# Optimization experiments

Measured on AMD Instinct MI355X. Metric: run time of the kernel, lower is better.

## Reference

```python
import jax, jax.numpy as jnp
import numpy as np

LN_EPS = 1e-5


def conv2d(x, w, b, stride, pad):
    # x: NCHW, w: OIHW
    y = jax.lax.conv_general_dilated(
        x, w, (stride, stride), [(pad, pad), (pad, pad)],
        dimension_numbers=("NCHW", "OIHW", "NCHW"))
    return y + b[None, :, None, None]


def gdn(x, gamma, beta):
    # y_c = x_c / sqrt(beta_c + sum_j gamma_cj * x_j^2)  (1x1 conv on x^2)
    norm = jnp.einsum("bchw,dc->bdhw", x * x, gamma) + beta[None, :, None, None]
    return x / jnp.sqrt(norm)


def layernorm(x, w, b):
    mu = jnp.mean(x, axis=-1, keepdims=True)
    var = jnp.var(x, axis=-1, keepdims=True)
    return (x - mu) / jnp.sqrt(var + LN_EPS) * w + b


def setup_inputs() -> dict:
    key = jax.random.key(0)
    ks = jax.random.split(key, 16)
    r = lambda i, shape: (jax.random.normal(ks[i], shape) * 0.02).astype(jnp.float32)
    N, M, K, D = 128, 192, 192, 128
    return {
        "x_p": jax.random.normal(ks[0], (4, 16, 3, 64, 64), jnp.float32),
        "y_g": jax.random.normal(ks[1], (64, K, 32), jnp.float32),
        "conv1_w": r(2, (N, 3, 5, 5)), "conv1_b": jnp.zeros((N,), jnp.float32),
        "gamma1": (0.1 * jnp.eye(N) + 1e-3).astype(jnp.float32), "beta1": jnp.ones((N,), jnp.float32),
        "conv2_w": r(3, (N, N, 5, 5)), "conv2_b": jnp.zeros((N,), jnp.float32),
        "gamma2": (0.1 * jnp.eye(N) + 1e-3).astype(jnp.float32), "beta2": jnp.ones((N,), jnp.float32),
        "conv3_w": r(4, (M, N, 3, 3)), "conv3_b": jnp.zeros((M,), jnp.float32),
        "ln_q_w": jnp.ones((M,), jnp.float32), "ln_q_b": jnp.zeros((M,), jnp.float32),
        "ln_kv_w": jnp.ones((K,), jnp.float32), "ln_kv_b": jnp.zeros((K,), jnp.float32),
        "ln_out_w": jnp.ones((M,), jnp.float32), "ln_out_b": jnp.zeros((M,), jnp.float32),
        "Wq": r(5, (D, M)), "Wk": r(6, (D, K)), "v_w": r(7, (1, D)),
        "Wv": r(8, (M, K)), "out_w": r(9, (M, M)), "out_b": jnp.zeros((M,), jnp.float32),
    }


def reference(x_p, y_g, conv1_w, conv1_b, gamma1, beta1, conv2_w, conv2_b,
              gamma2, beta2, conv3_w, conv3_b, ln_q_w, ln_q_b, ln_kv_w, ln_kv_b,
              ln_out_w, ln_out_b, Wq, Wk, v_w, Wv, out_w, out_b):
    B, P, C, Hp, Wp = x_p.shape
    x = x_p.reshape(B * P, C, Hp, Wp)
    # local encoder: conv s2 -> GDN -> conv s2 -> GDN -> conv s1 k3
    x = gdn(conv2d(x, conv1_w, conv1_b, 2, 2), gamma1, beta1)
    x = gdn(conv2d(x, conv2_w, conv2_b, 2, 2), gamma2, beta2)
    y_local = conv2d(x, conv3_w, conv3_b, 1, 1)          # (BP, M, h, w)
    BP, M, h, w = y_local.shape
    q = y_local.reshape(BP, M, h * w).transpose(0, 2, 1)  # (BP, Tq, M)
    kv = y_g.reshape(BP, y_g.shape[1], -1).transpose(0, 2, 1)  # (BP, Tk, K)
    q = layernorm(q, ln_q_w, ln_q_b)
    kv = layernorm(kv, ln_kv_w, ln_kv_b)
    # Bahdanau additive attention
    q_proj = jnp.einsum("bqm,dm->bqd", q, Wq)            # (BP, Tq, D)
    k_proj = jnp.einsum("bkc,dc->bkd", kv, Wk)           # (BP, Tk, D)
    energy = jnp.einsum("bqkd,d->bqk",
                        jnp.tanh(q_proj[:, :, None, :] + k_proj[:, None, :, :]),
                        v_w[0])                           # (BP, Tq, Tk)
    alpha = jax.nn.softmax(energy, axis=-1)
    v_proj = jnp.einsum("bkc,mc->bkm", kv, Wv)           # (BP, Tk, M)
    context = jnp.einsum("bqk,bkm->bqm", alpha, v_proj)
    context = jnp.einsum("bqm,nm->bqn", context, out_w) + out_b
    fused = layernorm(q + context, ln_out_w, ln_out_b)
    return fused.transpose(0, 2, 1).reshape(BP, M, h, w)
```

## Files before the change

### kernel.cpp

```cpp
#include <hip/hip_runtime.h>
#include <cstddef>
#include <cstdint>


typedef __bf16 bf16x8 __attribute__((ext_vector_type(8)));
typedef float floatx4 __attribute__((ext_vector_type(4)));
typedef unsigned short ushortT;
typedef unsigned short ushort8v __attribute__((ext_vector_type(8)));

#if __has_builtin(__builtin_amdgcn_exp2f)
#define EXP2F(x) __builtin_amdgcn_exp2f(x)
#else
#define EXP2F(x) exp2f(x)
#endif
#if __has_builtin(__builtin_amdgcn_rcpf)
#define RCPF(x) __builtin_amdgcn_rcpf(x)
#else
#define RCPF(x) (1.f / (x))
#endif

__device__ __forceinline__ ushortT f2bf(float f) {
  unsigned u = __builtin_bit_cast(unsigned, f);
  unsigned r = (u + 0x7FFFu + ((u >> 16) & 1u)) >> 16;
  return (ushortT)r;
}
__device__ __forceinline__ float bf2f(ushortT u) {
  return __builtin_bit_cast(float, ((unsigned)u) << 16);
}

static constexpr size_t OFF_T1BF = 0;
static constexpr size_t OFF_X2BF = 4194304;
static constexpr size_t OFF_T2BF = 8388608;
static constexpr size_t OFF_X3BF = 9437184;
static constexpr size_t OFF_QRAW = 10485760;
static constexpr size_t OFF_WBQ  = 21299200;
static constexpr size_t OFF_WBK  = 21311488;
static constexpr size_t OFF_WBV  = 21323776;
static constexpr size_t OFF_WBO  = 21342208;
static constexpr size_t OFF_WT2  = 26079232;
static constexpr size_t OFF_WT3  = 26284032;
static constexpr size_t OFF_WC1  = 26394624;
static constexpr size_t OFF_GB1  = 26406912;
static constexpr size_t OFF_GB2  = 26415104;

__device__ __constant__ int d_TWI2[4][9] = {{ 0, 2, 4,10,12,14,20,22,24},
                                            { 1, 3,11,13,21,23, 0, 0, 0},
                                            { 5, 7, 9,15,17,19, 0, 0, 0},
                                            { 6, 8,16,18, 0, 0, 0, 0, 0}};
__device__ __constant__ int d_NT2[4] = {9, 6, 6, 4};

__device__ void dev_convw3(const float* w, ushortT* wt, int mode, int total,
                           int idx) {
  if (idx >= total) return;
  int j    = idx & 7;
  int om   = (idx >> 3) & 63;
  int kg   = (idx >> 9) & 3;
  int slab = idx >> 11;
  int mt, s, tap, T;
  if (mode == 0) {
    int ph;
    if (slab < 72) ph = 0; else if (slab < 120) ph = 1;
    else if (slab < 168) ph = 2; else ph = 3;
    const int st[4] = {0, 72, 120, 168};
    const int ns[4] = {36, 24, 24, 16};
    int rel = slab - st[ph];
    mt = rel / ns[ph]; s = rel % ns[ph];
    tap = d_TWI2[ph][s >> 2]; T = 25;
  } else {
    mt = slab / 36; s = slab % 36; tap = s >> 2; T = 9;
  }
  int cc = s & 3;
  int c  = cc * 32 + kg * 8 + j;
  int oc = mt * 64 + om;
  wt[idx] = f2bf(w[(size_t)(oc * 128 + c) * T + tap]);
}

__device__ void dev_convw1(const float* w, ushortT* wt, int idx) {
  if (idx >= 20480) return;
  int k    = idx & 31;
  int oc   = (idx >> 5) & 127;
  int slab = idx >> 12;
  int ph, i;
  if (slab < 2) { ph = 0; i = slab; } else { ph = slab - 1; i = 0; }
  int kg = k >> 3, jj = k & 7;
  int tidx = i * 8 + jj;
  float val = 0.f;
  if (kg < 3 && tidx < d_NT2[ph]) {
    int tap = d_TWI2[ph][tidx];
    val = w[(size_t)(oc * 3 + kg) * 25 + tap];
  }
  wt[idx] = f2bf(val);
}

__device__ void dev_wcast(const float* w, ushortT* wb, int total, float scale,
                          int idx) {
  if (idx < total) wb[idx] = f2bf(w[idx] * scale);
}

__global__ __launch_bounds__(256) void prep_kernel(
    const float* __restrict__ conv2_w, ushortT* __restrict__ wt2,
    const float* __restrict__ conv3_w, ushortT* __restrict__ wt3,
    const float* __restrict__ conv1_w, ushortT* __restrict__ wc1,
    const float* __restrict__ Wq, ushortT* __restrict__ wbq,
    const float* __restrict__ Wk, ushortT* __restrict__ wbk,
    const float* __restrict__ Wv, ushortT* __restrict__ wbv,
    const float* __restrict__ out_w, ushortT* __restrict__ wbo,
    const float* __restrict__ gamma1, ushortT* __restrict__ gb1,
    const float* __restrict__ gamma2, ushortT* __restrict__ gb2) {
  constexpr float C2LE = 2.88539008177792681f;
  int blk = blockIdx.x, tid = threadIdx.x;
  if (blk < 1600)      dev_convw3(conv2_w, wt2, 0, 409600, blk * 256 + tid);
  else if (blk < 2464) dev_convw3(conv3_w, wt3, 1, 221184, (blk - 1600) * 256 + tid);
  else if (blk < 2544) dev_convw1(conv1_w, wc1, (blk - 2464) * 256 + tid);
  else if (blk < 2640) dev_wcast(Wq, wbq, 24576, C2LE, (blk - 2544) * 256 + tid);
  else if (blk < 2736) dev_wcast(Wk, wbk, 24576, C2LE, (blk - 2640) * 256 + tid);
  else if (blk < 2880) dev_wcast(Wv, wbv, 36864, 1.f, (blk - 2736) * 256 + tid);
  else if (blk < 3024) dev_wcast(out_w, wbo, 36864, 1.f, (blk - 2880) * 256 + tid);
  else if (blk < 3088) dev_wcast(gamma1, gb1, 16384, 1.f, (blk - 3024) * 256 + tid);
  else                 dev_wcast(gamma2, gb2, 16384, 1.f, (blk - 3088) * 256 + tid);
}

__global__ __launch_bounds__(256, 1) void conv1_mfma_kernel(
    const float* __restrict__ x, const ushortT* __restrict__ wc1,
    const float* __restrict__ bias, ushortT* __restrict__ outb) {
  int b  = blockIdx.x >> 2;
  int yg = blockIdx.x & 3;
  int y0 = yg * 8;

  int wave = threadIdx.x >> 6;
  int lane = threadIdx.x & 63;
  int ln15 = lane & 15;
  int kg   = lane >> 4;
  int tid  = threadIdx.x;

  __shared__ ushortT simg[4680];
  __shared__ ushortT sA[5 * 128 * 40];

  for (int j = tid; j < 2340; j += 256) ((unsigned*)simg)[j] = 0u;
  __syncthreads();

  int ihBase = 2 * y0 - 2;
  const float* xb = x + (size_t)b * 3 * 4096;
  for (int j = tid; j < 960; j += 256) {
    int q = j & 15;
    int rr = j >> 4;
    int c = rr / 20, ihl = rr % 20;
    int ih = ihBase + ihl;
    if (ih >= 0 && ih < 64) {
      float4 v = *(const float4*)&xb[c * 4096 + ih * 64 + q * 4];
      int pr = ih & 1, u = ih >> 1;
      int lr = u - y0 + 1;
      int base0 = ((pr * 2 + 0) * 3 + c) * 360 + lr * 36;
      int base1 = ((pr * 2 + 1) * 3 + c) * 360 + lr * 36;
      simg[base0 + 2 * q + 1] = f2bf(v.x);
      simg[base1 + 2 * q + 1] = f2bf(v.y);
      simg[base0 + 2 * q + 2] = f2bf(v.z);
      simg[base1 + 2 * q + 2] = f2bf(v.w);
    }
  }
  for (int j = tid; j < 2560; j += 256) {
    int chunk = j & 3, row = j >> 2;
    uint4 v = *(const uint4*)&wc1[row * 32 + chunk * 8];
    *(uint4*)&sA[row * 40 + chunk * 8] = v;
  }
  __syncthreads();

  constexpr int TDR[4][9] = {{-1,-1,-1, 0, 0, 0, 1, 1, 1},
                             {-1,-1, 0, 0, 1, 1, 0, 0, 0},
                             {-1,-1,-1, 0, 0, 0, 0, 0, 0},
                             {-1,-1, 0, 0, 0, 0, 0, 0, 0}};
  constexpr int TDC[4][9] = {{-1, 0, 1,-1, 0, 1,-1, 0, 1},
                             {-1, 0,-1, 0,-1, 0, 0, 0, 0},
                             {-1, 0, 1,-1, 0, 1, 0, 0, 0},
                             {-1, 0,-1, 0, 0, 0, 0, 0, 0}};
  constexpr int NT[4]  = {9, 6, 6, 4};
  constexpr int NM[4]  = {2, 1, 1, 1};
  constexpr int SB[4]  = {0, 2, 3, 4};

  ushort8v Bf[4][5];
  #pragma unroll
  for (int ntl = 0; ntl < 4; ++ntl) {
    int ntg = wave * 4 + ntl;
    int yloc = ntg >> 1;
    int xx = (ntg & 1) * 16 + ln15;
    int lbase = (yloc + 1) * 36 + xx + 1 + kg * 360;
    #pragma unroll
    for (int ph = 0; ph < 4; ++ph) {
      int pbase = ph * 1080 + lbase;
      #pragma unroll
      for (int i = 0; i < 2; ++i) {
        if (i < NM[ph]) {
          ushort8v bv;
          #pragma unroll
          for (int j = 0; j < 8; ++j) {
            int tidx = i * 8 + j;
            if (tidx >= NT[ph]) tidx = 0;
            int off = TDR[ph][tidx] * 36 + TDC[ph][tidx];
            bv[j] = simg[pbase + off];
          }
          Bf[ntl][SB[ph] + i] = bv;
        }
      }
    }
  }

  #pragma unroll
  for (int m = 0; m < 8; ++m) {
    bf16x8 Af[5];
    #pragma unroll
    for (int s = 0; s < 5; ++s)
      Af[s] = *(const bf16x8*)&sA[(s * 128 + m * 16 + ln15) * 40 + kg * 8];
    int oc0 = m * 16 + kg * 4;
    float4 bv = *(const float4*)&bias[oc0];
    #pragma unroll
    for (int ntl = 0; ntl < 4; ++ntl) {
      floatx4 acc = (floatx4)0.f;
      #pragma unroll
      for (int s = 0; s < 5; ++s)
        acc = __builtin_amdgcn_mfma_f32_16x16x32_bf16(
            Af[s], __builtin_bit_cast(bf16x8, Bf[ntl][s]), acc, 0, 0, 0);
      int ntg = wave * 4 + ntl;
      int y = y0 + (ntg >> 1);
      int xx = (ntg & 1) * 16 + ln15;
      int p = y * 32 + xx;
      ushort4 o4 = {f2bf(acc[0] + bv.x), f2bf(acc[1] + bv.y),
                    f2bf(acc[2] + bv.z), f2bf(acc[3] + bv.w)};
      *(ushort4*)&outb[((size_t)b * 1024 + p) * 128 + oc0] = o4;
    }
  }
}

__global__ __launch_bounds__(256) void gdn_mfma_kernel(
    const ushortT* __restrict__ xbf, const ushortT* __restrict__ gb,
    const float* __restrict__ beta, ushortT* __restrict__ ybf,
    int HW, int nPixTiles, int isSplit) {
  int pt = blockIdx.x % nPixTiles;
  int b  = blockIdx.x / nPixTiles;
  int px0 = pt * 64;
  int tid = threadIdx.x;
  int wave = tid >> 6, lane = tid & 63, ln15 = lane & 15, kg = lane >> 4;

  __shared__ ushortT sG[128 * 136];
  __shared__ ushortT sX[64 * 136];

  for (int j = tid; j < 2048; j += 256) {
    int row = j >> 4, ch = j & 15;
    *(uint4*)&sG[row * 136 + ch * 8] = *(const uint4*)&gb[row * 128 + ch * 8];
  }
  for (int j = tid; j < 1024; j += 256) {
    int row = j >> 4, ch = j & 15;
    ushort8v xv = *(const ushort8v*)&xbf[((size_t)(b * HW + px0 + row)) * 128 + ch * 8];
    ushort8v sq;
    #pragma unroll
    for (int r = 0; r < 8; ++r) {
      float f = bf2f(xv[r]);
      sq[r] = f2bf(f * f);
    }
    *(ushort8v*)&sX[row * 136 + ch * 8] = sq;
  }
  __syncthreads();

  floatx4 acc[2][4];
  #pragma unroll
  for (int mi = 0; mi < 2; ++mi)
    #pragma unroll
    for (int nt = 0; nt < 4; ++nt) acc[mi][nt] = (floatx4)0.f;

  #pragma unroll
  for (int k0 = 0; k0 < 128; k0 += 32) {
    bf16x8 a0 = *(const bf16x8*)&sG[(wave * 32 + ln15) * 136 + k0 + kg * 8];
    bf16x8 a1 = *(const bf16x8*)&sG[(wave * 32 + 16 + ln15) * 136 + k0 + kg * 8];
    #pragma unroll
    for (int nt = 0; nt < 4; ++nt) {
      bf16x8 bb = *(const bf16x8*)&sX[(nt * 16 + ln15) * 136 + k0 + kg * 8];
      acc[0][nt] = __builtin_amdgcn_mfma_f32_16x16x32_bf16(a0, bb, acc[0][nt], 0, 0, 0);
      acc[1][nt] = __builtin_amdgcn_mfma_f32_16x16x32_bf16(a1, bb, acc[1][nt], 0, 0, 0);
    }
  }

  #pragma unroll
  for (int mi = 0; mi < 2; ++mi) {
    int d0 = wave * 32 + mi * 16 + kg * 4;
    float4 bt = *(const float4*)&beta[d0];
    #pragma unroll
    for (int nt = 0; nt < 4; ++nt) {
      int p = px0 + nt * 16 + ln15;
      ushort4 x4 = *(const ushort4*)&xbf[((size_t)(b * HW + p)) * 128 + d0];
      ushort4 o4;
      o4.x = f2bf(bf2f(x4.x) * rsqrtf(acc[mi][nt][0] + bt.x));
      o4.y = f2bf(bf2f(x4.y) * rsqrtf(acc[mi][nt][1] + bt.y));
      o4.z = f2bf(bf2f(x4.z) * rsqrtf(acc[mi][nt][2] + bt.z));
      o4.w = f2bf(bf2f(x4.w) * rsqrtf(acc[mi][nt][3] + bt.w));
      size_t dst;
      if (isSplit) {
        int h = p >> 5, w5 = p & 31;
        int ph = ((h & 1) << 1) | (w5 & 1);
        dst = (((size_t)b * 4 + ph) * 256 + (h >> 1) * 16 + (w5 >> 1)) * 128 + d0;
      } else {
        dst = ((size_t)b * 256 + p) * 128 + d0;
      }
      *(ushort4*)&ybf[dst] = o4;
    }
  }
}

template<int MODE>
__global__ __launch_bounds__(256, 2) void conv_mfma_kernel(
    const ushortT* __restrict__ X,
    const ushortT* __restrict__ Wt,
    const float* __restrict__ bias,
    ushortT* __restrict__ outb) {
  constexpr int OC  = (MODE == 0) ? 128 : 192;
  constexpr int NMT = OC / 64;
  constexpr int NPH = (MODE == 0) ? 4 : 1;

  int b   = blockIdx.x / (NMT * 4);
  int rem = blockIdx.x % (NMT * 4);
  int mt  = rem >> 2;
  int rs  = rem & 3;
  int r0  = rs * 4;

  int wave = threadIdx.x >> 6;
  int lane = threadIdx.x & 63;
  int ln15 = lane & 15;
  int kg   = lane >> 4;

  __shared__ ushortT simg[6 * 18 * 136];

  floatx4 acc[4];
  #pragma unroll
  for (int m = 0; m < 4; ++m) acc[m] = (floatx4)0.f;

  constexpr int NS2[4]      = {36, 24, 24, 16};
  constexpr int PHSTART2[4] = {0, 72, 120, 168};
  constexpr int TDR_2[4][9] = {{-1,-1,-1, 0, 0, 0, 1, 1, 1},
                               {-1,-1, 0, 0, 1, 1, 0, 0, 0},
                               {-1,-1,-1, 0, 0, 0, 0, 0, 0},
                               {-1,-1, 0, 0, 0, 0, 0, 0, 0}};
  constexpr int TDC_2[4][9] = {{-1, 0, 1,-1, 0, 1,-1, 0, 1},
                               {-1, 0,-1, 0,-1, 0, 0, 0, 0},
                               {-1, 0, 1,-1, 0, 1, 0, 0, 0},
                               {-1, 0,-1, 0, 0, 0, 0, 0, 0}};
  constexpr int TDR_3[9] = {-1,-1,-1, 0, 0, 0, 1, 1, 1};
  constexpr int TDC_3[9] = {-1, 0, 1,-1, 0, 1,-1, 0, 1};

  const int aoff = kg * 512 + ln15 * 8;
  uint4 apf[8][4];

  #pragma unroll
  for (int ph = 0; ph < NPH; ++ph) {
    const int NS = (MODE == 0) ? NS2[ph] : 36;
    const int slabBase = (MODE == 0) ? (PHSTART2[ph] + mt * NS2[ph]) : (mt * 36);
    const ushortT* wp0 = Wt + (size_t)slabBase * 2048 + aoff;

    __syncthreads();
    const ushortT* Xb = X + (((size_t)b * NPH + ph) * 256) * 128;
    for (int idx = threadIdx.x; idx < 1728; idx += 256) {
      int chunk = idx & 15;
      int pix = idx >> 4;
      int row = pix / 18, colm = pix - row * 18;
      int i = r0 - 1 + row, j = colm - 1;
      uint4 v = {0u, 0u, 0u, 0u};
      if (i >= 0 && i < 16 && j >= 0 && j < 16)
        v = *(const uint4*)(Xb + ((size_t)(i * 16 + j)) * 128 + chunk * 8);
      *(uint4*)&simg[(row * 18 + colm) * 136 + chunk * 8] = v;
    }
    #pragma unroll
    for (int jj = 0; jj < 8; ++jj)
      if (jj < NS) {
        #pragma unroll
        for (int m = 0; m < 4; ++m)
          apf[jj][m] = *(const uint4*)(wp0 + (size_t)jj * 2048 + m * 128);
      }
    __syncthreads();

    #pragma unroll
    for (int s0 = 0; s0 < NS; s0 += 8) {
      #pragma unroll
      for (int jj = 0; jj < 8; ++jj) {
        int s = s0 + jj;
        if (s < NS) {
          bf16x8 acur[4];
          #pragma unroll
          for (int m = 0; m < 4; ++m) acur[m] = __builtin_bit_cast(bf16x8, apf[jj][m]);
          int sp = s + 8;
          if (sp < NS) {
            #pragma unroll
            for (int m = 0; m < 4; ++m)
              apf[jj][m] = *(const uint4*)(wp0 + (size_t)sp * 2048 + m * 128);
          }
          int t  = s >> 2;
          int c0 = (s & 3) * 32;
          int dr = (MODE == 0) ? TDR_2[ph][t] : TDR_3[t];
          int dc = (MODE == 0) ? TDC_2[ph][t] : TDC_3[t];
          int lrow = wave + dr + 1;
          int lcol = ln15 + dc + 1;
          bf16x8 bfr = *(const bf16x8*)&simg[(lrow * 18 + lcol) * 136 + c0 + kg * 8];
          #pragma unroll
          for (int m = 0; m < 4; ++m)
            acc[m] = __builtin_amdgcn_mfma_f32_16x16x32_bf16(acur[m], bfr, acc[m], 0, 0, 0);
        }
      }
    }
  }

  #pragma unroll
  for (int m = 0; m < 4; ++m) {
    int mg = mt * 64 + m * 16 + kg * 4;
    float4 bv = *(const float4*)&bias[mg];
    int r = r0 + wave;
    int p = r * 16 + ln15;
    ushort4 o4 = {f2bf(acc[m][0] + bv.x), f2bf(acc[m][1] + bv.y),
                  f2bf(acc[m][2] + bv.z), f2bf(acc[m][3] + bv.w)};
    *(ushort4*)&outb[((size_t)b * 256 + p) * OC + mg] = o4;
  }
}

__global__ __launch_bounds__(256) void attn_mega_kernel(
    const ushortT* __restrict__ qrawb, const float* __restrict__ ln_q_w,
    const float* __restrict__ ln_q_b, const float* __restrict__ yg,
    const float* __restrict__ ln_kv_w, const float* __restrict__ ln_kv_b,
    const ushortT* __restrict__ wbq, const ushortT* __restrict__ wbk,
    const ushortT* __restrict__ wbv, const ushortT* __restrict__ wbo,
    const float* __restrict__ vw, const float* __restrict__ out_b,
    const float* __restrict__ ln_out_w, const float* __restrict__ ln_out_b,
    float* __restrict__ out) {
  __shared__ ushortT smem[21762];
  ushortT* sqln = smem;
  ushortT* skv  = smem + 6400;
  ushortT* sqp  = smem + 12800;
  ushortT* skp  = smem + 17152;
  float*   swm  = (float*)(smem + 21504);
  float*   sS0  = (float*)(smem + 21760);
  ushortT* svp  = smem;
  float*   se   = (float*)(smem + 6400);
  ushortT* sctx = smem + 12800;
  float*   sf   = (float*)smem;

  int b  = blockIdx.x >> 3;
  int t0 = (blockIdx.x & 7) * 32;
  int tid  = threadIdx.x;
  int wave = tid >> 6;
  int lane = tid & 63;
  int ln15 = lane & 15;
  int kg   = lane >> 4;

  for (int r = wave; r < 32; r += 4) {
    const ushortT* xr = qrawb + ((size_t)(b * 256 + t0 + r)) * 192;
    float v0 = bf2f(xr[lane]), v1 = bf2f(xr[lane + 64]), v2 = bf2f(xr[lane + 128]);
    float s = v0 + v1 + v2;
    float s2 = v0 * v0 + v1 * v1 + v2 * v2;
    #pragma unroll
    for (int off = 32; off; off >>= 1) { s += __shfl_xor(s, off); s2 += __shfl_xor(s2, off); }
    float mean = s * (1.f / 192.f);
    float var = s2 * (1.f / 192.f) - mean * mean;
    float inv = rsqrtf(var + 1e-5f);
    sqln[r * 200 + lane]       = f2bf((v0 - mean) * inv * ln_q_w[lane]       + ln_q_b[lane]);
    sqln[r * 200 + lane + 64]  = f2bf((v1 - mean) * inv * ln_q_w[lane + 64]  + ln_q_b[lane + 64]);
    sqln[r * 200 + lane + 128] = f2bf((v2 - mean) * inv * ln_q_w[lane + 128] + ln_q_b[lane + 128]);
  }
  for (int r = wave; r < 32; r += 4) {
    const float* src = yg + (size_t)b * 6144 + r;
    float v0 = src[(size_t)lane * 32];
    float v1 = src[(size_t)(lane + 64) * 32];
    float v2 = src[(size_t)(lane + 128) * 32];
    float s = v0 + v1 + v2;
    float s2 = v0 * v0 + v1 * v1 + v2 * v2;
    #pragma unroll
    for (int off = 32; off; off >>= 1) { s += __shfl_xor(s, off); s2 += __shfl_xor(s2, off); }
    float mean = s * (1.f / 192.f);
    float var = s2 * (1.f / 192.f) - mean * mean;
    float inv = rsqrtf(var + 1e-5f);
    skv[r * 200 + lane]       = f2bf((v0 - mean) * inv * ln_kv_w[lane]       + ln_kv_b[lane]);
    skv[r * 200 + lane + 64]  = f2bf((v1 - mean) * inv * ln_kv_w[lane + 64]  + ln_kv_b[lane + 64]);
    skv[r * 200 + lane + 128] = f2bf((v2 - mean) * inv * ln_kv_w[lane + 128] + ln_kv_b[lane + 128]);
  }
  __syncthreads();

  for (int ti = wave; ti < 16; ti += 4) {
    int rt = ti >> 3, ct = ti & 7;
    floatx4 acc = (floatx4)0.f;
    #pragma unroll
    for (int k0 = 0; k0 < 192; k0 += 32) {
      bf16x8 afr = *(const bf16x8*)&sqln[(rt * 16 + ln15) * 200 + k0 + kg * 8];
      bf16x8 bfr = *(const bf16x8*)&wbq[((size_t)(ct * 16 + ln15)) * 192 + k0 + kg * 8];
      acc = __builtin_amdgcn_mfma_f32_16x16x32_bf16(afr, bfr, acc, 0, 0, 0);
    }
    #pragma unroll
    for (int r = 0; r < 4; ++r)
      sqp[(rt * 16 + kg * 4 + r) * 136 + ct * 16 + ln15] = f2bf(acc[r]);
  }
  for (int ti = wave; ti < 16; ti += 4) {
    int rt = ti >> 3, ct = ti & 7;
    floatx4 acc = (floatx4)0.f;
    #pragma unroll
    for (int k0 = 0; k0 < 192; k0 += 32) {
      bf16x8 afr = *(const bf16x8*)&skv[(rt * 16 + ln15) * 200 + k0 + kg * 8];
      bf16x8 bfr = *(const bf16x8*)&wbk[((size_t)(ct * 16 + ln15)) * 192 + k0 + kg * 8];
      acc = __builtin_amdgcn_mfma_f32_16x16x32_bf16(afr, bfr, acc, 0, 0, 0);
    }
    #pragma unroll
    for (int r = 0; r < 4; ++r)
      skp[(rt * 16 + kg * 4 + r) * 136 + ct * 16 + ln15] = f2bf(acc[r]);
  }
  __syncthreads();

  for (int ti = wave; ti < 24; ti += 4) {
    int rt = ti / 12, ct = ti % 12;
    floatx4 acc = (floatx4)0.f;
    #pragma unroll
    for (int k0 = 0; k0 < 192; k0 += 32) {
      bf16x8 afr = *(const bf16x8*)&skv[(rt * 16 + ln15) * 200 + k0 + kg * 8];
      bf16x8 bfr = *(const bf16x8*)&wbv[((size_t)(ct * 16 + ln15)) * 192 + k0 + kg * 8];
      acc = __builtin_amdgcn_mfma_f32_16x16x32_bf16(afr, bfr, acc, 0, 0, 0);
    }
    #pragma unroll
    for (int r = 0; r < 4; ++r)
      svp[(rt * 16 + kg * 4 + r) * 200 + ct * 16 + ln15] = f2bf(acc[r]);
  }
  if (tid < 128) swm[tid] = -2.f * vw[tid];
  if (tid < 64) {
    float s = vw[tid] + vw[tid + 64];
    #pragma unroll
    for (int off = 32; off; off >>= 1) s += __shfl_xor(s, off);
    if (tid == 0) *sS0 = s;
  }
  __syncthreads();

  {
    float S0v = *sS0;
    int qq0 = tid >> 4, kc = tid & 15;
    const float4* w4 = (const float4*)swm;
    #pragma unroll
    for (int st = 0; st < 2; ++st) {
      int qq = st * 16 + qq0;
      const ushortT* qrow = sqp + qq * 136;
      const ushortT* kr0 = skp + kc * 136;
      const ushortT* kr1 = skp + (kc + 16) * 136;
      float acc0 = S0v, acc1 = S0v;
      #pragma unroll 8
      for (int d4 = 0; d4 < 32; ++d4) {
        ushort4 qu = *(const ushort4*)&qrow[d4 * 4];
        ushort4 k0u = *(const ushort4*)&kr0[d4 * 4];
        ushort4 k1u = *(const ushort4*)&kr1[d4 * 4];
        float4 wv = w4[d4];
        float qx = bf2f(qu.x), qy = bf2f(qu.y), qz = bf2f(qu.z), qw = bf2f(qu.w);
        acc0 += wv.x * RCPF(EXP2F(qx + bf2f(k0u.x)) + 1.f);
        acc0 += wv.y * RCPF(EXP2F(qy + bf2f(k0u.y)) + 1.f);
        acc0 += wv.z * RCPF(EXP2F(qz + bf2f(k0u.z)) + 1.f);
        acc0 += wv.w * RCPF(EXP2F(qw + bf2f(k0u.w)) + 1.f);
        acc1 += wv.x * RCPF(EXP2F(qx + bf2f(k1u.x)) + 1.f);
        acc1 += wv.y * RCPF(EXP2F(qy + bf2f(k1u.y)) + 1.f);
        acc1 += wv.z * RCPF(EXP2F(qz + bf2f(k1u.z)) + 1.f);
        acc1 += wv.w * RCPF(EXP2F(qw + bf2f(k1u.w)) + 1.f);
      }
      se[qq * 33 + kc] = acc0;
      se[qq * 33 + kc + 16] = acc1;
    }
  }
  __syncthreads();

  if (tid < 32) {
    float* ser = se + tid * 33;
    float mx = -1e30f;
    for (int k = 0; k < 32; ++k) mx = fmaxf(mx, ser[k]);
    float s = 0.f;
    for (int k = 0; k < 32; ++k) { float a = __expf(ser[k] - mx); ser[k] = a; s += a; }
    float invs = 1.f / s;
    for (int k = 0; k < 32; ++k) ser[k] *= invs;
  }
  __syncthreads();

  for (int j = tid; j < 1536; j += 256) {
    int qq = j / 48, m4 = j % 48;
    const float* al = se + qq * 33;
    float4 a = {0.f, 0.f, 0.f, 0.f};
    #pragma unroll 8
    for (int k = 0; k < 32; ++k) {
      float wk = al[k];
      ushort4 vv = *(const ushort4*)&svp[k * 200 + m4 * 4];
      a.x += wk * bf2f(vv.x); a.y += wk * bf2f(vv.y);
      a.z += wk * bf2f(vv.z); a.w += wk * bf2f(vv.w);
    }
    ushort4 o4 = {f2bf(a.x), f2bf(a.y), f2bf(a.z), f2bf(a.w)};
    *(ushort4*)&sctx[qq * 200 + m4 * 4] = o4;
  }
  __syncthreads();

  for (int ti = wave; ti < 24; ti += 4) {
    int rt = ti / 12, ct = ti % 12;
    floatx4 acc = (floatx4)0.f;
    #pragma unroll
    for (int k0 = 0; k0 < 192; k0 += 32) {
      bf16x8 afr = *(const bf16x8*)&sctx[(rt * 16 + ln15) * 200 + k0 + kg * 8];
      bf16x8 bfr = *(const bf16x8*)&wbo[((size_t)(ct * 16 + ln15)) * 192 + k0 + kg * 8];
      acc = __builtin_amdgcn_mfma_f32_16x16x32_bf16(afr, bfr, acc, 0, 0, 0);
    }
    float bv = out_b[ct * 16 + ln15];
    #pragma unroll
    for (int r = 0; r < 4; ++r)
      sf[(rt * 16 + kg * 4 + r) * 193 + ct * 16 + ln15] = acc[r] + bv;
  }
  __syncthreads();

  for (int rr = wave; rr < 32; rr += 4) {
    int t = t0 + rr;
    const ushortT* xr = qrawb + ((size_t)(b * 256 + t)) * 192;
    float r0_ = bf2f(xr[lane]), r1_ = bf2f(xr[lane + 64]), r2_ = bf2f(xr[lane + 128]);
    float s = r0_ + r1_ + r2_;
    float s2 = r0_ * r0_ + r1_ * r1_ + r2_ * r2_;
    #pragma unroll
    for (int off = 32; off; off >>= 1) { s += __shfl_xor(s, off); s2 += __shfl_xor(s2, off); }
    float mean = s * (1.f / 192.f);
    float var = s2 * (1.f / 192.f) - mean * mean;
    float inv = rsqrtf(var + 1e-5f);
    float q0 = (r0_ - mean) * inv * ln_q_w[lane]       + ln_q_b[lane];
    float q1 = (r1_ - mean) * inv * ln_q_w[lane + 64]  + ln_q_b[lane + 64];
    float q2 = (r2_ - mean) * inv * ln_q_w[lane + 128] + ln_q_b[lane + 128];
    float v0 = sf[rr * 193 + lane]       + q0;
    float v1 = sf[rr * 193 + lane + 64]  + q1;
    float v2 = sf[rr * 193 + lane + 128] + q2;
    float t_s = v0 + v1 + v2;
    float t_s2 = v0 * v0 + v1 * v1 + v2 * v2;
    #pragma unroll
    for (int off = 32; off; off >>= 1) { t_s += __shfl_xor(t_s, off); t_s2 += __shfl_xor(t_s2, off); }
    float m2 = t_s * (1.f / 192.f);
    float var2 = t_s2 * (1.f / 192.f) - m2 * m2;
    float inv2 = rsqrtf(var2 + 1e-5f);
    sf[rr * 193 + lane]       = (v0 - m2) * inv2 * ln_out_w[lane]       + ln_out_b[lane];
    sf[rr * 193 + lane + 64]  = (v1 - m2) * inv2 * ln_out_w[lane + 64]  + ln_out_b[lane + 64];
    sf[rr * 193 + lane + 128] = (v2 - m2) * inv2 * ln_out_w[lane + 128] + ln_out_b[lane + 128];
  }
  __syncthreads();

  for (int j = tid; j < 1536; j += 256) {
    int m = j >> 3, t4 = j & 7;
    float4 o4;
    o4.x = sf[(t4 * 4 + 0) * 193 + m];
    o4.y = sf[(t4 * 4 + 1) * 193 + m];
    o4.z = sf[(t4 * 4 + 2) * 193 + m];
    o4.w = sf[(t4 * 4 + 3) * 193 + m];
    *(float4*)&out[((size_t)(b * 192 + m)) * 256 + t0 + t4 * 4] = o4;
  }
}

extern "C" void kernel_launch(void* const* d_in, const int* in_sizes, int n_in,
                              void* d_out, int out_size, void* d_ws, size_t ws_size,
                              hipStream_t stream) {
  (void)in_sizes; (void)n_in; (void)out_size; (void)ws_size;
  const float* x_p     = (const float*)d_in[0];
  const float* y_g     = (const float*)d_in[1];
  const float* conv1_w = (const float*)d_in[2];
  const float* conv1_b = (const float*)d_in[3];
  const float* gamma1  = (const float*)d_in[4];
  const float* beta1   = (const float*)d_in[5];
  const float* conv2_w = (const float*)d_in[6];
  const float* conv2_b = (const float*)d_in[7];
  const float* gamma2  = (const float*)d_in[8];
  const float* beta2   = (const float*)d_in[9];
  const float* conv3_w = (const float*)d_in[10];
  const float* conv3_b = (const float*)d_in[11];
  const float* ln_q_w  = (const float*)d_in[12];
  const float* ln_q_b  = (const float*)d_in[13];
  const float* ln_kv_w = (const float*)d_in[14];
  const float* ln_kv_b = (const float*)d_in[15];
  const float* ln_out_w= (const float*)d_in[16];
  const float* ln_out_b= (const float*)d_in[17];
  const float* Wq      = (const float*)d_in[18];
  const float* Wk      = (const float*)d_in[19];
  const float* v_w     = (const float*)d_in[20];
  const float* Wv      = (const float*)d_in[21];
  const float* out_w   = (const float*)d_in[22];
  const float* out_b   = (const float*)d_in[23];
  float* out = (float*)d_out;
  float* ws  = (float*)d_ws;

  ushortT* t1bf  = (ushortT*)(ws + OFF_T1BF);
  ushortT* x2bf  = (ushortT*)(ws + OFF_X2BF);
  ushortT* t2bf  = (ushortT*)(ws + OFF_T2BF);
  ushortT* x3bf  = (ushortT*)(ws + OFF_X3BF);
  ushortT* qrawb = (ushortT*)(ws + OFF_QRAW);
  ushortT* wbq   = (ushortT*)(ws + OFF_WBQ);
  ushortT* wbk   = (ushortT*)(ws + OFF_WBK);
  ushortT* wbv   = (ushortT*)(ws + OFF_WBV);
  ushortT* wbo   = (ushortT*)(ws + OFF_WBO);
  ushortT* wt2   = (ushortT*)(ws + OFF_WT2);
  ushortT* wt3   = (ushortT*)(ws + OFF_WT3);
  ushortT* wc1   = (ushortT*)(ws + OFF_WC1);
  ushortT* gb1   = (ushortT*)(ws + OFF_GB1);
  ushortT* gb2   = (ushortT*)(ws + OFF_GB2);

  prep_kernel<<<3152, 256, 0, stream>>>(conv2_w, wt2, conv3_w, wt3, conv1_w, wc1,
                                        Wq, wbq, Wk, wbk, Wv, wbv, out_w, wbo,
                                        gamma1, gb1, gamma2, gb2);
  conv1_mfma_kernel<<<256, 256, 0, stream>>>(x_p, wc1, conv1_b, t1bf);
  gdn_mfma_kernel<<<1024, 256, 0, stream>>>(t1bf, gb1, beta1, x2bf, 1024, 16, 1);
  conv_mfma_kernel<0><<<512, 256, 0, stream>>>(x2bf, wt2, conv2_b, t2bf);
  gdn_mfma_kernel<<<256, 256, 0, stream>>>(t2bf, gb2, beta2, x3bf, 256, 4, 0);
  conv_mfma_kernel<1><<<768, 256, 0, stream>>>(x3bf, wt3, conv3_b, qrawb);
  attn_mega_kernel<<<512, 256, 0, stream>>>(qrawb, ln_q_w, ln_q_b, y_g,
                                            ln_kv_w, ln_kv_b, wbq, wbk, wbv,
                                            wbo, v_w, out_b, ln_out_w,
                                            ln_out_b, out);
}
```

Measured before the change: 262.8 us.

## Restructure attention kernel: stage y_g coalesced, merge projections, MFMA for context

The attention kernel now loads y_g with coalesced float4 reads into a transposed shared buffer before the KV layernorm, instead of making strided global reads. The Q, K and V projections are merged into one 56-tile loop under a single barrier. The Q and K projections are kept in fp32 so the tanh loop no longer converts from bf16. The alpha·V context product now uses one bf16 MFMA per tile against a transposed V buffer rather than scalar FMAs. Shared memory grows from about 43KB to about 75KB, which may lower occupancy. Alpha is also rounded to bf16 before the multiply.

```diff
diff --git a/kernel.cpp b/kernel.cpp
--- a/kernel.cpp
+++ b/kernel.cpp
@@ -425,17 +425,18 @@
     const float* __restrict__ vw, const float* __restrict__ out_b,
     const float* __restrict__ ln_out_w, const float* __restrict__ ln_out_b,
     float* __restrict__ out) {
-  __shared__ ushortT smem[21762];
-  ushortT* sqln = smem;
-  ushortT* skv  = smem + 6400;
-  ushortT* sqp  = smem + 12800;
-  ushortT* skp  = smem + 17152;
-  float*   swm  = (float*)(smem + 21504);
-  float*   sS0  = (float*)(smem + 21760);
-  ushortT* svp  = smem;
-  float*   se   = (float*)(smem + 6400);
-  ushortT* sctx = smem + 12800;
-  float*   sf   = (float*)smem;
+  __shared__ ushortT smem[37640];
+  ushortT* sqln   = smem;
+  ushortT* skv    = smem + 6400;
+  float*   skvRaw = (float*)(smem + 12800);
+  float*   sqpF   = (float*)(smem + 12800);
+  float*   skpF   = (float*)(smem + 21248);
+  ushortT* svpT   = smem + 29696;
+  float*   swm    = (float*)(smem + 37376);
+  float*   sS0    = (float*)(smem + 37632);
+  float*   se     = (float*)(smem + 6400);
+  ushortT* sctx   = smem + 12800;
+  float*   sf     = (float*)(smem + 21248);
 
   int b  = blockIdx.x >> 3;
   int t0 = (blockIdx.x & 7) * 32;
@@ -445,6 +446,18 @@
   int ln15 = lane & 15;
   int kg   = lane >> 4;
 
+  {
+    const float4* yg4 = (const float4*)(yg + (size_t)b * 6144);
+    for (int j = tid; j < 1536; j += 256) {
+      float4 v = yg4[j];
+      int c = j >> 3;
+      int t4 = (j & 7) * 4;
+      skvRaw[(t4 + 0) * 194 + c] = v.x;
+      skvRaw[(t4 + 1) * 194 + c] = v.y;
+      skvRaw[(t4 + 2) * 194 + c] = v.z;
+      skvRaw[(t4 + 3) * 194 + c] = v.w;
+    }
+  }
   for (int r = wave; r < 32; r += 4) {
     const ushortT* xr = qrawb + ((size_t)(b * 256 + t0 + r)) * 192;
     float v0 = bf2f(xr[lane]), v1 = bf2f(xr[lane + 64]), v2 = bf2f(xr[lane + 128]);
@@ -459,11 +472,19 @@
     sqln[r * 200 + lane + 64]  = f2bf((v1 - mean) * inv * ln_q_w[lane + 64]  + ln_q_b[lane + 64]);
     sqln[r * 200 + lane + 128] = f2bf((v2 - mean) * inv * ln_q_w[lane + 128] + ln_q_b[lane + 128]);
   }
+  if (tid < 128) swm[tid] = -2.f * vw[tid];
+  if (tid >= 128 && tid < 192) {
+    int l = tid - 128;
+    float s = vw[l] + vw[l + 64];
+    #pragma unroll
+    for (int off = 32; off; off >>= 1) s += __shfl_xor(s, off);
+    if (l == 0) *sS0 = s;
+  }
+  __syncthreads();
+
   for (int r = wave; r < 32; r += 4) {
-    const float* src = yg + (size_t)b * 6144 + r;
-    float v0 = src[(size_t)lane * 32];
-    float v1 = src[(size_t)(lane + 64) * 32];
-    float v2 = src[(size_t)(lane + 128) * 32];
+    const float* src = skvRaw + r * 194;
+    float v0 = src[lane], v1 = src[lane + 64], v2 = src[lane + 128];
     float s = v0 + v1 + v2;
     float s2 = v0 * v0 + v1 * v1 + v2 * v2;
     #pragma unroll
@@ -477,53 +498,44 @@
   }
   __syncthreads();
 
-  for (int ti = wave; ti < 16; ti += 4) {
-    int rt = ti >> 3, ct = ti & 7;
+  for (int ti = wave; ti < 56; ti += 4) {
     floatx4 acc = (floatx4)0.f;
-    #pragma unroll
-    for (int k0 = 0; k0 < 192; k0 += 32) {
-      bf16x8 afr = *(const bf16x8*)&sqln[(rt * 16 + ln15) * 200 + k0 + kg * 8];
-      bf16x8 bfr = *(const bf16x8*)&wbq[((size_t)(ct * 16 + ln15)) * 192 + k0 + kg * 8];
-      acc = __builtin_amdgcn_mfma_f32_16x16x32_bf16(afr, bfr, acc, 0, 0, 0);
-    }
-    #pragma unroll
-    for (int r = 0; r < 4; ++r)
-      sqp[(rt * 16 + kg * 4 + r) * 136 + ct * 16 + ln15] = f2bf(acc[r]);
-  }
-  for (int ti = wave; ti < 16; ti += 4) {
-    int rt = ti >> 3, ct = ti & 7;
-    floatx4 acc = (floatx4)0.f;
-    #pragma unroll
-    for (int k0 = 0; k0 < 192; k0 += 32) {
-      bf16x8 afr = *(const bf16x8*)&skv[(rt * 16 + ln15) * 200 + k0 + kg * 8];
-      bf16x8 bfr = *(const bf16x8*)&wbk[((size_t)(ct * 16 + ln15)) * 192 + k0 + kg * 8];
-      acc = __builtin_amdgcn_mfma_f32_16x16x32_bf16(afr, bfr, acc, 0, 0, 0);
-    }
-    #pragma unroll
-    for (int r = 0; r < 4; ++r)
-      skp[(rt * 16 + kg * 4 + r) * 136 + ct * 16 + ln15] = f2bf(acc[r]);
-  }
-  __syncthreads();
-
-  for (int ti = wave; ti < 24; ti += 4) {
-    int rt = ti / 12, ct = ti % 12;
-    floatx4 acc = (floatx4)0.f;
-    #pragma unroll
-    for (int k0 = 0; k0 < 192; k0 += 32) {
-      bf16x8 afr = *(const bf16x8*)&skv[(rt * 16 + ln15) * 200 + k0 + kg * 8];
-      bf16x8 bfr = *(const bf16x8*)&wbv[((size_t)(ct * 16 + ln15)) * 192 + k0 + kg * 8];
-      acc = __builtin_amdgcn_mfma_f32_16x16x32_bf16(afr, bfr, acc, 0, 0, 0);
-    }
-    #pragma unroll
-    for (int r = 0; r < 4; ++r)
-      svp[(rt * 16 + kg * 4 + r) * 200 + ct * 16 + ln15] = f2bf(acc[r]);
-  }
-  if (tid < 128) swm[tid] = -2.f * vw[tid];
-  if (tid < 64) {
-    float s = vw[tid] + vw[tid + 64];
-    #pragma unroll
-    for (int off = 32; off; off >>= 1) s += __shfl_xor(s, off);
-    if (tid == 0) *sS0 = s;
+    if (ti < 16) {
+      int rt = ti >> 3, ct = ti & 7;
+      #pragma unroll
+      for (int k0 = 0; k0 < 192; k0 += 32) {
+        bf16x8 afr = *(const bf16x8*)&sqln[(rt * 16 + ln15) * 200 + k0 + kg * 8];
+        bf16x8 bfr = *(const bf16x8*)&wbq[((size_t)(ct * 16 + ln15)) * 192 + k0 + kg * 8];
+        acc = __builtin_amdgcn_mfma_f32_16x16x32_bf16(afr, bfr, acc, 0, 0, 0);
+      }
+      #pragma unroll
+      for (int r = 0; r < 4; ++r)
+        sqpF[(rt * 16 + kg * 4 + r) * 132 + ct * 16 + ln15] = acc[r];
+    } else if (ti < 32) {
+      int t2 = ti - 16;
+      int rt = t2 >> 3, ct = t2 & 7;
+      #pragma unroll
+      for (int k0 = 0; k0 < 192; k0 += 32) {
+        bf16x8 afr = *(const bf16x8*)&skv[(rt * 16 + ln15) * 200 + k0 + kg * 8];
+        bf16x8 bfr = *(const bf16x8*)&wbk[((size_t)(ct * 16 + ln15)) * 192 + k0 + kg * 8];
+        acc = __builtin_amdgcn_mfma_f32_16x16x32_bf16(afr, bfr, acc, 0, 0, 0);
+      }
+      #pragma unroll
+      for (int r = 0; r < 4; ++r)
+        skpF[(rt * 16 + kg * 4 + r) * 132 + ct * 16 + ln15] = acc[r];
+    } else {
+      int t2 = ti - 32;
+      int rt = t2 / 12, ct = t2 % 12;
+      #pragma unroll
+      for (int k0 = 0; k0 < 192; k0 += 32) {
+        bf16x8 afr = *(const bf16x8*)&skv[(rt * 16 + ln15) * 200 + k0 + kg * 8];
+        bf16x8 bfr = *(const bf16x8*)&wbv[((size_t)(ct * 16 + ln15)) * 192 + k0 + kg * 8];
+        acc = __builtin_amdgcn_mfma_f32_16x16x32_bf16(afr, bfr, acc, 0, 0, 0);
+      }
+      #pragma unroll
+      for (int r = 0; r < 4; ++r)
+        svpT[(ct * 16 + ln15) * 40 + rt * 16 + kg * 4 + r] = f2bf(acc[r]);
+    }
   }
   __syncthreads();
 
@@ -534,34 +546,30 @@
     #pragma unroll
     for (int st = 0; st < 2; ++st) {
       int qq = st * 16 + qq0;
-      const ushortT* qrow = sqp + qq * 136;
-      const ushortT* kr0 = skp + kc * 136;
-      const ushortT* kr1 = skp + (kc + 16) * 136;
+      const float4* q4 = (const float4*)&sqpF[qq * 132];
+      const float4* ka = (const float4*)&skpF[kc * 132];
+      const float4* kb = (const float4*)&skpF[(kc + 16) * 132];
       float acc0 = S0v, acc1 = S0v;
       #pragma unroll 8
       for (int d4 = 0; d4 < 32; ++d4) {
-        ushort4 qu = *(const ushort4*)&qrow[d4 * 4];
-        ushort4 k0u = *(const ushort4*)&kr0[d4 * 4];
-        ushort4 k1u = *(const ushort4*)&kr1[d4 * 4];
-        float4 wv = w4[d4];
-        float qx = bf2f(qu.x), qy = bf2f(qu.y), qz = bf2f(qu.z), qw = bf2f(qu.w);
-        acc0 += wv.x * RCPF(EXP2F(qx + bf2f(k0u.x)) + 1.f);
-        acc0 += wv.y * RCPF(EXP2F(qy + bf2f(k0u.y)) + 1.f);
-        acc0 += wv.z * RCPF(EXP2F(qz + bf2f(k0u.z)) + 1.f);
-        acc0 += wv.w * RCPF(EXP2F(qw + bf2f(k0u.w)) + 1.f);
-        acc1 += wv.x * RCPF(EXP2F(qx + bf2f(k1u.x)) + 1.f);
-        acc1 += wv.y * RCPF(EXP2F(qy + bf2f(k1u.y)) + 1.f);
-        acc1 += wv.z * RCPF(EXP2F(qz + bf2f(k1u.z)) + 1.f);
-        acc1 += wv.w * RCPF(EXP2F(qw + bf2f(k1u.w)) + 1.f);
+        float4 qv = q4[d4], k0v = ka[d4], k1v = kb[d4], wv = w4[d4];
+        acc0 += wv.x * RCPF(EXP2F(qv.x + k0v.x) + 1.f);
+        acc0 += wv.y * RCPF(EXP2F(qv.y + k0v.y) + 1.f);
+        acc0 += wv.z * RCPF(EXP2F(qv.z + k0v.z) + 1.f);
+        acc0 += wv.w * RCPF(EXP2F(qv.w + k0v.w) + 1.f);
+        acc1 += wv.x * RCPF(EXP2F(qv.x + k1v.x) + 1.f);
+        acc1 += wv.y * RCPF(EXP2F(qv.y + k1v.y) + 1.f);
+        acc1 += wv.z * RCPF(EXP2F(qv.z + k1v.z) + 1.f);
+        acc1 += wv.w * RCPF(EXP2F(qv.w + k1v.w) + 1.f);
       }
-      se[qq * 33 + kc] = acc0;
-      se[qq * 33 + kc + 16] = acc1;
+      se[qq * 36 + kc] = acc0;
+      se[qq * 36 + kc + 16] = acc1;
     }
   }
   __syncthreads();
 
   if (tid < 32) {
-    float* ser = se + tid * 33;
+    float* ser = se + tid * 36;
     float mx = -1e30f;
     for (int k = 0; k < 32; ++k) mx = fmaxf(mx, ser[k]);
     float s = 0.f;
@@ -571,19 +579,19 @@
   }
   __syncthreads();
 
-  for (int j = tid; j < 1536; j += 256) {
-    int qq = j / 48, m4 = j % 48;
-    const float* al = se + qq * 33;
-    float4 a = {0.f, 0.f, 0.f, 0.f};
-    #pragma unroll 8
-    for (int k = 0; k < 32; ++k) {
-      float wk = al[k];
-      ushort4 vv = *(const ushort4*)&svp[k * 200 + m4 * 4];
-      a.x += wk * bf2f(vv.x); a.y += wk * bf2f(vv.y);
-      a.z += wk * bf2f(vv.z); a.w += wk * bf2f(vv.w);
-    }
-    ushort4 o4 = {f2bf(a.x), f2bf(a.y), f2bf(a.z), f2bf(a.w)};
-    *(ushort4*)&sctx[qq * 200 + m4 * 4] = o4;
+  for (int ti = wave; ti < 24; ti += 4) {
+    int rt = ti / 12, ct = ti % 12;
+    float4 a0 = *(const float4*)&se[(rt * 16 + ln15) * 36 + kg * 8];
+    float4 a1 = *(const float4*)&se[(rt * 16 + ln15) * 36 + kg * 8 + 4];
+    ushort8v au;
+    au[0] = f2bf(a0.x); au[1] = f2bf(a0.y); au[2] = f2bf(a0.z); au[3] = f2bf(a0.w);
+    au[4] = f2bf(a1.x); au[5] = f2bf(a1.y); au[6] = f2bf(a1.z); au[7] = f2bf(a1.w);
+    bf16x8 bfr = *(const bf16x8*)&svpT[(ct * 16 + ln15) * 40 + kg * 8];
+    floatx4 acc = __builtin_amdgcn_mfma_f32_16x16x32_bf16(
+        __builtin_bit_cast(bf16x8, au), bfr, (floatx4)0.f, 0, 0, 0);
+    #pragma unroll
+    for (int r = 0; r < 4; ++r)
+      sctx[(rt * 16 + kg * 4 + r) * 200 + ct * 16 + ln15] = f2bf(acc[r]);
   }
   __syncthreads();
 
```

Measured after the change: 254.1 us. 1.03x faster.
